# Performance work log

Measured on AMD Instinct MI355X. Metric: run time of the kernel, lower is better.

The kernel has to match this reference:

```python
import jax, jax.numpy as jnp
import numpy as np

EPS = 1e-6
K = 16
TEMP = 1.0
RES_SCALE = 0.5
CLAMP_MAX = 50.0


def _knn_indices(x, k):
    # x: (B,N,3) -> idx (B,N,k), self excluded; squared dist preserves ordering
    sq = jnp.sum(x * x, axis=-1)                      # (B,N)
    d2 = sq[:, :, None] + sq[:, None, :] - 2.0 * jnp.einsum('bnd,bmd->bnm', x, x)
    N = x.shape[1]
    eye = jnp.eye(N, dtype=bool)
    d2 = jnp.where(eye[None], jnp.inf, d2)
    _, idx = jax.lax.top_k(-d2, k)
    return idx


def _gather(t, idx):
    # t: (B,N,...), idx: (B,N,k) -> (B,N,k,...)
    return jax.vmap(lambda tb, ib: tb[ib])(t, idx)


def _vn_linear(v, W):
    return jnp.einsum('bncd,oc->bnod', v, W)


def _edge_mlp(s, W1, b1, W2, b2, W3, b3):
    h = jax.nn.silu(s @ W1.T + b1)
    h = jax.nn.silu(h @ W2.T + b2)
    return h @ W3.T + b3


def _vn_layer_norm(x, gamma, beta):
    norm = jnp.maximum(jnp.linalg.norm(x, axis=-1), EPS)      # (B,N,C)
    mean = jnp.mean(norm, axis=-1, keepdims=True)
    std = jnp.maximum(jnp.std(norm, axis=-1, keepdims=True, ddof=1), EPS)
    norm_scaled = (norm - mean) / std * gamma + beta
    return x / norm[..., None] * jnp.maximum(norm_scaled[..., None], EPS)


def _clamp_features(x, max_norm):
    n = jnp.maximum(jnp.linalg.norm(x, axis=-1, keepdims=True), EPS)
    scale = jnp.minimum(max_norm / n, 1.0)
    return x * scale


def setup_inputs() -> dict:
    key = jax.random.key(0)
    ks = jax.random.split(key, 12)
    B, N, C, Cout, H = 8, 2048, 128, 128, 32
    gain = 0.5
    lim = gain * np.sqrt(6.0 / (C + Cout))
    inp = {
        'x': jax.random.normal(ks[0], (B, N, 3), jnp.float32),
        'v': jax.random.normal(ks[1], (B, N, C, 3), jnp.float32),
        'Wq': jax.random.uniform(ks[2], (Cout, C), jnp.float32, -lim, lim),
        'Wk': jax.random.uniform(ks[3], (Cout, C), jnp.float32, -lim, lim),
        'Wu': jax.random.uniform(ks[4], (Cout, C), jnp.float32, -lim, lim),
        'W1': jax.random.normal(ks[5], (H, 4), jnp.float32) * 0.3,
        'b1': jnp.zeros((H,), jnp.float32),
        'W2': jax.random.normal(ks[6], (H, H), jnp.float32) * 0.15,
        'b2': jnp.zeros((H,), jnp.float32),
        'W3': jax.random.normal(ks[7], (1, H), jnp.float32) * 0.15,
        'b3': jnp.zeros((1,), jnp.float32),
        'gamma': jnp.ones((Cout,), jnp.float32),
        'beta': jnp.zeros((Cout,), jnp.float32),
    }
    return inp


def reference(x, v, Wq, Wk, Wu, W1, b1, W2, b2, W3, b3, gamma, beta):
    idx = _knn_indices(jax.lax.stop_gradient(x), K)           # (B,N,k)
    x_nbr = _gather(x, idx)                                    # (B,N,k,3)
    Q = _vn_linear(v, Wq)                                      # (B,N,Co,3)
    Kt = _vn_linear(v, Wk)
    U = _vn_linear(v, Wu)
    K_nbr = _gather(Kt, idx)                                   # (B,N,k,Co,3)
    U_nbr = _gather(U, idx)
    qn = jnp.mean(jnp.linalg.norm(Q, axis=-1), axis=-1, keepdims=True)   # (B,N,1)
    kn = jnp.mean(jnp.linalg.norm(Kt, axis=-1), axis=-1, keepdims=True)
    kn_nbr = _gather(kn, idx)                                  # (B,N,k,1)
    dot_nbr = jnp.mean(jnp.sum(Q[:, :, None] * K_nbr, axis=-1), axis=-1, keepdims=True)  # (B,N,k,1)
    dist = jnp.linalg.norm(x[:, :, None] - x_nbr, axis=-1, keepdims=True)                # (B,N,k,1)
    qn_exp = jnp.broadcast_to(qn[:, :, None], kn_nbr.shape)
    edge_s = jnp.concatenate([qn_exp, kn_nbr, dot_nbr, dist], axis=-1)   # (B,N,k,4)
    logits = jnp.clip(_edge_mlp(edge_s, W1, b1, W2, b2, W3, b3) / TEMP, -10.0, 10.0)
    attn = jax.nn.softmax(logits, axis=2)                      # (B,N,k,1)
    msg = jnp.sum(attn[..., None] * U_nbr, axis=2)             # (B,N,Co,3)
    out = Q + RES_SCALE * msg
    out = _vn_layer_norm(out, gamma, beta)
    out = _clamp_features(out, CLAMP_MAX)
    return out
```

## Files before the change

kernel.cpp:

```cpp
#include <hip/hip_runtime.h>
#include <math.h>

#define BB 8
#define NN 2048
#define CC 128
#define KNB 16
#define BN (BB*NN)
#define WPAD 136

#define EMPTYK 0xFFFFFFFFFFFFFFFFULL

typedef __attribute__((ext_vector_type(8))) short short8;
typedef __attribute__((ext_vector_type(4))) float floatx4;
typedef __attribute__((ext_vector_type(4), aligned(4))) float floatx4u;

__device__ __forceinline__ float silu_f(float x) {
  const float e = __builtin_amdgcn_exp2f(-1.442695040888963f * x);
  return x * __builtin_amdgcn_rcpf(1.0f + e);
}
__device__ __forceinline__ float fsqrt(float x) { return __builtin_amdgcn_sqrtf(x); }
__device__ __forceinline__ float frcp(float x)  { return __builtin_amdgcn_rcpf(x); }

__device__ __forceinline__ unsigned long long umin64(unsigned long long a, unsigned long long b) {
  return (b < a) ? b : a;
}

__device__ __forceinline__ unsigned short f2bf(float f) {
  unsigned u = __float_as_uint(f);
  unsigned r = u + 0x7FFFu + ((u >> 16) & 1u);
  return (unsigned short)(r >> 16);
}
__device__ __forceinline__ float bf2f(unsigned short s) {
  return __uint_as_float(((unsigned)s) << 16);
}

__device__ __forceinline__ float dot8(const float* __restrict__ w, const float* __restrict__ h) {
  const float4 a = *(const float4*)w;
  const float4 b = *(const float4*)(w + 4);
  float s = a.x*h[0];
  s = fmaf(a.y, h[1], s); s = fmaf(a.z, h[2], s); s = fmaf(a.w, h[3], s);
  s = fmaf(b.x, h[4], s); s = fmaf(b.y, h[5], s); s = fmaf(b.z, h[6], s);
  s = fmaf(b.w, h[7], s);
  return s;
}

__global__ __launch_bounds__(256) void knn_kernel(const float* __restrict__ x,
                                                  int* __restrict__ idx) {
  const int lane = threadIdx.x & 63;
  const int wave = threadIdx.x >> 6;
  const int bn = blockIdx.x * 4 + wave;
  const int b = bn >> 11;
  const int n = bn & (NN - 1);

  const float* xb = x + (size_t)b * NN * 3;
  const double xn0 = (double)xb[n*3+0], xn1 = (double)xb[n*3+1], xn2 = (double)xb[n*3+2];
  const double sqn = xn0*xn0 + xn1*xn1 + xn2*xn2;

  unsigned long long k[32];
  unsigned long long t0 = EMPTYK, t1 = EMPTYK, t2 = EMPTYK, t3 = EMPTYK;

  #pragma unroll
  for (int i = 0; i < 32; ++i) {
    const int m = i*64 + lane;
    const double a0 = (double)xb[m*3+0], a1 = (double)xb[m*3+1], a2 = (double)xb[m*3+2];
    const double sqm = a0*a0 + a1*a1 + a2*a2;
    const double dot = xn0*a0 + xn1*a1 + xn2*a2;
    const double d = sqn + sqm - 2.0*dot;
    unsigned long long kk =
        ((unsigned long long)__double_as_longlong(d) & ~2047ULL) | (unsigned long long)m;
    if (m == n) kk = 0x8000000000000000ULL | (unsigned long long)m;
    k[i] = kk;
    const bool l3 = kk < t3, l2 = kk < t2, l1 = kk < t1, l0 = kk < t0;
    t3 = l3 ? (l2 ? t2 : kk) : t3;
    t2 = l2 ? (l1 ? t1 : kk) : t2;
    t1 = l1 ? (l0 ? t0 : kk) : t1;
    t0 = l0 ? kk : t0;
  }

  int* op = idx + (size_t)bn * KNB;
  for (int t = 0; t < KNB; ++t) {
    unsigned long long g = t0;
    #pragma unroll
    for (int off = 32; off > 0; off >>= 1)
      g = umin64(g, (unsigned long long)__shfl_xor((unsigned long long)g, off, 64));

    if (lane == 0) op[t] = (int)(g & 2047ULL);

    const bool own = (t0 == g);
    t0 = own ? t1 : t0;
    t1 = own ? t2 : t1;
    t2 = own ? t3 : t2;
    t3 = own ? EMPTYK : t3;

    const bool need = (t0 == EMPTYK);
    if (__any(need)) {
      unsigned long long nm = EMPTYK;
      #pragma unroll
      for (int i = 0; i < 32; ++i) {
        const unsigned long long c = (k[i] > g) ? k[i] : EMPTYK;
        nm = umin64(nm, c);
      }
      t0 = need ? nm : t0;
    }
  }
}

__global__ __launch_bounds__(256) void wconv_kernel(
    const float* __restrict__ Wq, const float* __restrict__ Wk, const float* __restrict__ Wu,
    unsigned short* __restrict__ Whl)
{
  const int i = blockIdx.x*256 + threadIdx.x;
  const int mat = i >> 14, rem = i & 16383;
  const float* W = (mat == 0) ? Wq : ((mat == 1) ? Wk : Wu);
  const float f = W[rem];
  const unsigned short h = f2bf(f);
  const float r = f - bf2f(h);
  unsigned short* base = Whl + (size_t)mat * 2 * CC * CC;
  base[rem]           = h;
  base[CC*CC + rem]   = f2bf(r);
}

__global__ __launch_bounds__(256, 2) void vn_gemm_mfma(
    const float* __restrict__ v, const unsigned short* __restrict__ Whl,
    float* __restrict__ Q, float* __restrict__ Kt, float* __restrict__ U)
{
  __shared__ short Wh[CC][WPAD];
  __shared__ short Wl[CC][WPAD];

  const int tid  = threadIdx.x;
  const int lane = tid & 63;
  const int wave = tid >> 6;
  const int quad = lane >> 4;
  const int l15  = lane & 15;

  const int m = blockIdx.x*64 + wave*16 + l15;
  const int p = m / 3, d = m - 3*p;
  const float* vb = v + (size_t)p * (CC*3) + d;
  float areg[32];
  #pragma unroll
  for (int kc = 0; kc < 4; ++kc)
    #pragma unroll
    for (int j = 0; j < 8; ++j)
      areg[kc*8+j] = vb[(kc*32 + quad*8 + j)*3];

  short8 ah[4], al[4];
  #pragma unroll
  for (int kc = 0; kc < 4; ++kc)
    #pragma unroll
    for (int j = 0; j < 8; ++j) {
      const float f = areg[kc*8+j];
      unsigned short h = f2bf(f);
      float r = f - bf2f(h);
      ah[kc][j] = (short)h;
      al[kc][j] = (short)f2bf(r);
    }

  const int r0s = blockIdx.x*64 + wave*16 + quad*4;
  int pbase[4];
  #pragma unroll
  for (int reg = 0; reg < 4; ++reg) {
    const int r = r0s + reg;
    const int pp = r / 3;
    pbase[reg] = pp * (CC*3) + (r - 3*pp);
  }
  const int l153 = l15 * 3;

  for (int mat = 0; mat < 3; ++mat) {
    float* __restrict__ Out = (mat == 0) ? Q : ((mat == 1) ? Kt : U);
    const unsigned short* Wg = Whl + (size_t)mat * 2 * CC * CC;

    #pragma unroll
    for (int it = 0; it < 8; ++it) {
      const int i = it*256 + tid;
      const int o = i >> 4, c8 = (i & 15) * 8;
      *(short8*)&Wh[o][c8] = *(const short8*)&Wg[o*CC + c8];
      *(short8*)&Wl[o][c8] = *(const short8*)&Wg[CC*CC + o*CC + c8];
    }
    __syncthreads();

    floatx4 acc[8];
    #pragma unroll
    for (int ct = 0; ct < 8; ++ct) acc[ct] = (floatx4){0.f, 0.f, 0.f, 0.f};

    #pragma unroll
    for (int kc = 0; kc < 4; ++kc) {
      #pragma unroll
      for (int ct = 0; ct < 8; ++ct) {
        const int o = ct*16 + l15;
        const short8 bh = *(const short8*)&Wh[o][kc*32 + quad*8];
        const short8 bl = *(const short8*)&Wl[o][kc*32 + quad*8];
        acc[ct] = __builtin_amdgcn_mfma_f32_16x16x32_bf16(ah[kc], bh, acc[ct], 0, 0, 0);
        acc[ct] = __builtin_amdgcn_mfma_f32_16x16x32_bf16(al[kc], bh, acc[ct], 0, 0, 0);
        acc[ct] = __builtin_amdgcn_mfma_f32_16x16x32_bf16(ah[kc], bl, acc[ct], 0, 0, 0);
      }
    }
    __syncthreads();

    #pragma unroll
    for (int ct = 0; ct < 8; ++ct) {
      const int o3 = ct*48 + l153;
      #pragma unroll
      for (int reg = 0; reg < 4; ++reg)
        Out[pbase[reg] + o3] = acc[ct][reg];
    }
  }
}

__global__ __launch_bounds__(256) void kn_kernel(const float* __restrict__ Kt,
                                                 float* __restrict__ kn) {
  const int lane = threadIdx.x & 63;
  const int wave = threadIdx.x >> 6;
  const int bn = blockIdx.x * 4 + wave;
  const float* Kp = Kt + (size_t)bn * (CC*3) + lane*6;
  const floatx4u a = *(const floatx4u*)Kp;
  const float2 c = *(const float2*)(Kp+4);
  float s = fsqrt(a.x*a.x + a.y*a.y + a.z*a.z) + fsqrt(a.w*a.w + c.x*c.x + c.y*c.y);
  #pragma unroll
  for (int off = 1; off < 64; off <<= 1) s += __shfl_xor(s, off, 64);
  if (lane == 0) kn[bn] = s * (1.0f/128.0f);
}

__global__ __launch_bounds__(256) void attn_wave_kernel(
    const float* __restrict__ x, const int* __restrict__ idx,
    const float* __restrict__ Q, const float* __restrict__ Kt, const float* __restrict__ U,
    const float* __restrict__ kn,
    const float* __restrict__ W1, const float* __restrict__ b1,
    const float* __restrict__ W2, const float* __restrict__ b2,
    const float* __restrict__ W3, const float* __restrict__ b3,
    const float* __restrict__ gam, const float* __restrict__ bet,
    float* __restrict__ out)
{
  const int lane = threadIdx.x & 63;
  const int wv   = threadIdx.x >> 6;
  const int bn = ((blockIdx.x & 7) << 11) | (((blockIdx.x >> 3) << 2) | wv);
  const int b = bn >> 11;

  const float* Qp = Q + (size_t)bn * (CC*3) + lane*6;
  const floatx4u q0 = *(const floatx4u*)Qp;
  const float2 q1 = *(const float2*)(Qp+4);
  const float2 qa = make_float2(q0.x, q0.y);
  const float2 qb = make_float2(q0.z, q0.w);
  const float2 qc = make_float2(q1.x, q1.y);

  const int* ip = idx + (size_t)bn * KNB;
  int j[KNB];
  #pragma unroll
  for (int t = 0; t < KNB; ++t) j[t] = ip[t];

  const int kk = lane & 15;
  int jsel = j[0];
  #pragma unroll
  for (int t = 1; t < KNB; ++t) jsel = (kk == t) ? j[t] : jsel;

  const float xi0 = x[(size_t)bn*3+0], xi1 = x[(size_t)bn*3+1], xi2 = x[(size_t)bn*3+2];
  const float* xj = x + (size_t)(b*NN + jsel)*3;
  const float xj0 = xj[0], xj1 = xj[1], xj2 = xj[2];
  const float s1 = kn[(size_t)b*NN + jsel];

  float dpart[KNB];
  #pragma unroll
  for (int t = 0; t < KNB; ++t) {
    const float* Kp = Kt + (size_t)(b*NN + j[t]) * (CC*3) + lane*6;
    const floatx4u kv = *(const floatx4u*)Kp;
    const float2 kw = *(const float2*)(Kp+4);
    dpart[t] = qa.x*kv.x + qa.y*kv.y + qb.x*kv.z + qb.y*kv.w + qc.x*kw.x + qc.y*kw.y;
  }
  float qnp = fsqrt(qa.x*qa.x + qa.y*qa.y + qb.x*qb.x) + fsqrt(qb.y*qb.y + qc.x*qc.x + qc.y*qc.y);

  #pragma unroll
  for (int off = 1; off < 64; off <<= 1) qnp += __shfl_xor(qnp, off, 64);
  const float s0 = qnp * (1.0f/128.0f);

  float d8[8];
  {
    const bool hb = (lane & 1) != 0;
    #pragma unroll
    for (int t = 0; t < 8; ++t) {
      const float keep = hb ? dpart[2*t+1] : dpart[2*t];
      const float send = hb ? dpart[2*t]   : dpart[2*t+1];
      d8[t] = keep + __shfl_xor(send, 1, 64);
    }
  }
  float d4[4];
  {
    const bool hb = (lane & 2) != 0;
    #pragma unroll
    for (int t = 0; t < 4; ++t) {
      const float keep = hb ? d8[2*t+1] : d8[2*t];
      const float send = hb ? d8[2*t]   : d8[2*t+1];
      d4[t] = keep + __shfl_xor(send, 2, 64);
    }
  }
  float d2[2];
  {
    const bool hb = (lane & 4) != 0;
    #pragma unroll
    for (int t = 0; t < 2; ++t) {
      const float keep = hb ? d4[2*t+1] : d4[2*t];
      const float send = hb ? d4[2*t]   : d4[2*t+1];
      d2[t] = keep + __shfl_xor(send, 4, 64);
    }
  }
  float dsel;
  {
    const bool hb = (lane & 8) != 0;
    const float keep = hb ? d2[1] : d2[0];
    const float send = hb ? d2[0] : d2[1];
    dsel = keep + __shfl_xor(send, 8, 64);
  }
  dsel += __shfl_xor(dsel, 16, 64);
  dsel += __shfl_xor(dsel, 32, 64);

  const float dx = xi0 - xj0, dy = xi1 - xj1, dz = xi2 - xj2;
  const float s3 = fsqrt(dx*dx + dy*dy + dz*dz);
  const float s2 = dsel * (1.0f/128.0f);

  float u0[KNB], u1[KNB], u2[KNB], u3[KNB], u4[KNB], u5[KNB];
  #pragma unroll
  for (int t = 0; t < KNB; ++t) {
    const float* Up = U + (size_t)(b*NN + j[t]) * (CC*3) + lane*6;
    const floatx4u uv = *(const floatx4u*)Up;
    const float2 uw = *(const float2*)(Up+4);
    u0[t]=uv.x; u1[t]=uv.y; u2[t]=uv.z; u3[t]=uv.w; u4[t]=uw.x; u5[t]=uw.y;
  }

  const int g = lane >> 4;
  const int o0 = g*8, o1 = (g^1)*8, o2 = (g^2)*8, o3 = (g^3)*8;

  float h1o[8];
  {
    const float4 b1a = *(const float4*)(b1 + o0);
    const float4 b1b = *(const float4*)(b1 + o0 + 4);
    const float bb1[8] = {b1a.x,b1a.y,b1a.z,b1a.w,b1b.x,b1b.y,b1b.z,b1b.w};
    #pragma unroll
    for (int jj = 0; jj < 8; ++jj) {
      const float4 w = *(const float4*)(W1 + (o0 + jj)*4);
      float u = bb1[jj];
      u = fmaf(w.x, s0, u); u = fmaf(w.y, s1, u);
      u = fmaf(w.z, s2, u); u = fmaf(w.w, s3, u);
      h1o[jj] = silu_f(u);
    }
  }
  float hx16[8], hx32[8], hx48[8];
  #pragma unroll
  for (int jj = 0; jj < 8; ++jj) hx16[jj] = __shfl_xor(h1o[jj], 16, 64);
  #pragma unroll
  for (int jj = 0; jj < 8; ++jj) hx32[jj] = __shfl_xor(h1o[jj], 32, 64);
  #pragma unroll
  for (int jj = 0; jj < 8; ++jj) hx48[jj] = __shfl_xor(hx16[jj], 32, 64);

  float logit;
  {
    const float4 b2a = *(const float4*)(b2 + o0);
    const float4 b2b = *(const float4*)(b2 + o0 + 4);
    const float bb2[8] = {b2a.x,b2a.y,b2a.z,b2a.w,b2b.x,b2b.y,b2b.z,b2b.w};
    const float4 w3a = *(const float4*)(W3 + o0);
    const float4 w3b = *(const float4*)(W3 + o0 + 4);
    const float ww3[8] = {w3a.x,w3a.y,w3a.z,w3a.w,w3b.x,w3b.y,w3b.z,w3b.w};
    float lp = 0.f;
    #pragma unroll
    for (int hh = 0; hh < 8; ++hh) {
      const float* wr = W2 + (o0 + hh)*32;
      float a = bb2[hh];
      a += dot8(wr + o0, h1o);
      a += dot8(wr + o1, hx16);
      a += dot8(wr + o2, hx32);
      a += dot8(wr + o3, hx48);
      lp = fmaf(ww3[hh], silu_f(a), lp);
    }
    lp += __shfl_xor(lp, 16, 64);
    lp += __shfl_xor(lp, 32, 64);
    logit = lp + b3[0];
  }
  logit = fminf(fmaxf(logit, -10.0f), 10.0f);

  float mx = logit;
  #pragma unroll
  for (int off = 8; off > 0; off >>= 1) mx = fmaxf(mx, __shfl_xor(mx, off, 16));
  const float e = __builtin_amdgcn_exp2f(1.442695040888963f * (logit - mx));
  float ssum = e;
  #pragma unroll
  for (int off = 8; off > 0; off >>= 1) ssum += __shfl_xor(ssum, off, 16);
  const float w = e * frcp(ssum);

  float wk[KNB];
  #pragma unroll
  for (int t = 0; t < KNB; ++t) wk[t] = __shfl(w, t, 64);

  float m0=0.f,m1=0.f,m2=0.f,m3=0.f,m4=0.f,m5=0.f;
  #pragma unroll
  for (int t = 0; t < KNB; ++t) {
    const float ww = wk[t];
    m0 = fmaf(ww, u0[t], m0); m1 = fmaf(ww, u1[t], m1); m2 = fmaf(ww, u2[t], m2);
    m3 = fmaf(ww, u3[t], m3); m4 = fmaf(ww, u4[t], m4); m5 = fmaf(ww, u5[t], m5);
  }
  const float oa0 = qa.x + 0.5f*m0, oa1 = qa.y + 0.5f*m1, oa2 = qb.x + 0.5f*m2;
  const float ob0 = qb.y + 0.5f*m3, ob1 = qc.x + 0.5f*m4, ob2 = qc.y + 0.5f*m5;

  const float na = fmaxf(fsqrt(oa0*oa0 + oa1*oa1 + oa2*oa2), 1e-6f);
  const float nb = fmaxf(fsqrt(ob0*ob0 + ob1*ob1 + ob2*ob2), 1e-6f);
  float s = na + nb;
  #pragma unroll
  for (int off = 1; off < 64; off <<= 1) s += __shfl_xor(s, off, 64);
  const float mean = s * (1.0f/128.0f);
  const float dva = na - mean, dvb = nb - mean;
  float s2v = dva*dva + dvb*dvb;
  #pragma unroll
  for (int off = 1; off < 64; off <<= 1) s2v += __shfl_xor(s2v, off, 64);
  const float stdv = fmaxf(fsqrt(s2v * (1.0f/127.0f)), 1e-6f);
  const float rstd = frcp(stdv);

  const float2 gm = *(const float2*)(gam + lane*2);
  const float2 bt = *(const float2*)(bet + lane*2);
  const float nsa = (na - mean) * rstd * gm.x + bt.x;
  const float nsb = (nb - mean) * rstd * gm.y + bt.y;
  const float sca = fmaxf(nsa, 1e-6f) * frcp(na);
  const float scb = fmaxf(nsb, 1e-6f) * frcp(nb);
  float fa0 = oa0*sca, fa1 = oa1*sca, fa2 = oa2*sca;
  float fb0 = ob0*scb, fb1 = ob1*scb, fb2 = ob2*scb;
  const float n2a = fmaxf(fsqrt(fa0*fa0 + fa1*fa1 + fa2*fa2), 1e-6f);
  const float n2b = fmaxf(fsqrt(fb0*fb0 + fb1*fb1 + fb2*fb2), 1e-6f);
  const float c2a = fminf(50.0f * frcp(n2a), 1.0f);
  const float c2b = fminf(50.0f * frcp(n2b), 1.0f);

  float* op = out + (size_t)bn * (CC*3) + lane*6;
  floatx4u o4; o4.x = fa0*c2a; o4.y = fa1*c2a; o4.z = fa2*c2a; o4.w = fb0*c2b;
  *(floatx4u*)op = o4;
  *(float2*)(op+4) = make_float2(fb1*c2b, fb2*c2b);
}

extern "C" void kernel_launch(void* const* d_in, const int* in_sizes, int n_in,
                              void* d_out, int out_size, void* d_ws, size_t ws_size,
                              hipStream_t stream) {
  (void)in_sizes; (void)n_in; (void)out_size; (void)ws_size;
  const float* x   = (const float*)d_in[0];
  const float* v   = (const float*)d_in[1];
  const float* Wq  = (const float*)d_in[2];
  const float* Wk  = (const float*)d_in[3];
  const float* Wu  = (const float*)d_in[4];
  const float* W1  = (const float*)d_in[5];
  const float* b1  = (const float*)d_in[6];
  const float* W2  = (const float*)d_in[7];
  const float* b2  = (const float*)d_in[8];
  const float* W3  = (const float*)d_in[9];
  const float* b3  = (const float*)d_in[10];
  const float* gam = (const float*)d_in[11];
  const float* bet = (const float*)d_in[12];
  float* out = (float*)d_out;

  char* ws = (char*)d_ws;
  int*   idx = (int*)ws;
  float* Q   = (float*)(ws + (size_t)BN * KNB * 4);
  float* Kt  = Q  + (size_t)BN * CC * 3;
  float* U   = Kt + (size_t)BN * CC * 3;
  unsigned short* Whl = (unsigned short*)(U + (size_t)BN * CC * 3);
  float* kn  = (float*)((char*)Whl + (size_t)3 * 2 * CC * CC * 2);

  knn_kernel<<<BN/4, 256, 0, stream>>>(x, idx);
  wconv_kernel<<<192, 256, 0, stream>>>(Wq, Wk, Wu, Whl);
  vn_gemm_mfma<<<(BN*3)/64, 256, 0, stream>>>(v, Whl, Q, Kt, U);
  kn_kernel<<<BN/4, 256, 0, stream>>>(Kt, kn);
  attn_wave_kernel<<<BN/4, 256, 0, stream>>>(x, idx, Q, Kt, U, kn,
                                             W1, b1, W2, b2, W3, b3, gam, bet, out);
}
```

Baseline: 279.3 us.

## Split attention into logits and message kernels, fuse kn into logits, cheapen knn argmin

Removes the standalone kn kernel and instead computes neighbor key norms on the fly from the K rows already loaded for the dot products. The attention kernel is split in two: one computes softmax weights into a workspace array, the other gathers U and does the weighted sum plus layer norm. This lowers register pressure from holding 96 U values per lane. The knn top-k selection replaces the 64-bit shuffle min with a 32-bit high-word reduction plus a ballot, and only falls back to a low-word reduction when the high words tie. In exchange, Q and idx are read twice and the weights take an extra global round trip.

```diff
diff --git a/kernel.cpp b/kernel.cpp
--- a/kernel.cpp
+++ b/kernel.cpp
@@ -79,14 +79,33 @@
 
   int* op = idx + (size_t)bn * KNB;
   for (int t = 0; t < KNB; ++t) {
-    unsigned long long g = t0;
-    #pragma unroll
-    for (int off = 32; off > 0; off >>= 1)
-      g = umin64(g, (unsigned long long)__shfl_xor((unsigned long long)g, off, 64));
-
-    if (lane == 0) op[t] = (int)(g & 2047ULL);
-
-    const bool own = (t0 == g);
+    const unsigned h0 = (unsigned)(t0 >> 32);
+    const unsigned l0w = (unsigned)t0;
+    unsigned hm = h0;
+    #pragma unroll
+    for (int off = 32; off > 0; off >>= 1) {
+      const unsigned o = (unsigned)__shfl_xor((int)hm, off, 64);
+      hm = (o < hm) ? o : hm;
+    }
+    const bool tied = (h0 == hm);
+    const unsigned long long bal = __ballot(tied);
+    unsigned lm;
+    if (__builtin_popcountll(bal) == 1) {
+      const int owner = __builtin_ctzll(bal);
+      lm = (unsigned)__shfl((int)l0w, owner, 64);
+    } else {
+      lm = tied ? l0w : 0xFFFFFFFFu;
+      #pragma unroll
+      for (int off = 32; off > 0; off >>= 1) {
+        const unsigned o = (unsigned)__shfl_xor((int)lm, off, 64);
+        lm = (o < lm) ? o : lm;
+      }
+    }
+    const unsigned long long g = ((unsigned long long)hm << 32) | (unsigned long long)lm;
+
+    if (lane == 0) op[t] = (int)(lm & 2047u);
+
+    const bool own = tied && (l0w == lm);
     t0 = own ? t1 : t0;
     t1 = own ? t2 : t1;
     t2 = own ? t3 : t2;
@@ -206,29 +225,13 @@
   }
 }
 
-__global__ __launch_bounds__(256) void kn_kernel(const float* __restrict__ Kt,
-                                                 float* __restrict__ kn) {
-  const int lane = threadIdx.x & 63;
-  const int wave = threadIdx.x >> 6;
-  const int bn = blockIdx.x * 4 + wave;
-  const float* Kp = Kt + (size_t)bn * (CC*3) + lane*6;
-  const floatx4u a = *(const floatx4u*)Kp;
-  const float2 c = *(const float2*)(Kp+4);
-  float s = fsqrt(a.x*a.x + a.y*a.y + a.z*a.z) + fsqrt(a.w*a.w + c.x*c.x + c.y*c.y);
-  #pragma unroll
-  for (int off = 1; off < 64; off <<= 1) s += __shfl_xor(s, off, 64);
-  if (lane == 0) kn[bn] = s * (1.0f/128.0f);
-}
-
-__global__ __launch_bounds__(256) void attn_wave_kernel(
+__global__ __launch_bounds__(256) void attn_logits_kernel(
     const float* __restrict__ x, const int* __restrict__ idx,
-    const float* __restrict__ Q, const float* __restrict__ Kt, const float* __restrict__ U,
-    const float* __restrict__ kn,
+    const float* __restrict__ Q, const float* __restrict__ Kt,
     const float* __restrict__ W1, const float* __restrict__ b1,
     const float* __restrict__ W2, const float* __restrict__ b2,
     const float* __restrict__ W3, const float* __restrict__ b3,
-    const float* __restrict__ gam, const float* __restrict__ bet,
-    float* __restrict__ out)
+    float* __restrict__ warr)
 {
   const int lane = threadIdx.x & 63;
   const int wv   = threadIdx.x >> 6;
@@ -255,15 +258,15 @@
   const float xi0 = x[(size_t)bn*3+0], xi1 = x[(size_t)bn*3+1], xi2 = x[(size_t)bn*3+2];
   const float* xj = x + (size_t)(b*NN + jsel)*3;
   const float xj0 = xj[0], xj1 = xj[1], xj2 = xj[2];
-  const float s1 = kn[(size_t)b*NN + jsel];
-
-  float dpart[KNB];
+
+  float dpart[KNB], knp[KNB];
   #pragma unroll
   for (int t = 0; t < KNB; ++t) {
     const float* Kp = Kt + (size_t)(b*NN + j[t]) * (CC*3) + lane*6;
     const floatx4u kv = *(const floatx4u*)Kp;
     const float2 kw = *(const float2*)(Kp+4);
     dpart[t] = qa.x*kv.x + qa.y*kv.y + qb.x*kv.z + qb.y*kv.w + qc.x*kw.x + qc.y*kw.y;
+    knp[t] = fsqrt(kv.x*kv.x + kv.y*kv.y + kv.z*kv.z) + fsqrt(kv.w*kv.w + kw.x*kw.x + kw.y*kw.y);
   }
   float qnp = fsqrt(qa.x*qa.x + qa.y*qa.y + qb.x*qb.x) + fsqrt(qb.y*qb.y + qc.x*qc.x + qc.y*qc.y);
 
@@ -271,58 +274,67 @@
   for (int off = 1; off < 64; off <<= 1) qnp += __shfl_xor(qnp, off, 64);
   const float s0 = qnp * (1.0f/128.0f);
 
-  float d8[8];
+  float d8[8], k8[8];
   {
     const bool hb = (lane & 1) != 0;
     #pragma unroll
     for (int t = 0; t < 8; ++t) {
-      const float keep = hb ? dpart[2*t+1] : dpart[2*t];
-      const float send = hb ? dpart[2*t]   : dpart[2*t+1];
-      d8[t] = keep + __shfl_xor(send, 1, 64);
-    }
-  }
-  float d4[4];
+      const float dk = hb ? dpart[2*t+1] : dpart[2*t];
+      const float dsn = hb ? dpart[2*t]  : dpart[2*t+1];
+      const float kv = hb ? knp[2*t+1]   : knp[2*t];
+      const float ksn = hb ? knp[2*t]    : knp[2*t+1];
+      d8[t] = dk + __shfl_xor(dsn, 1, 64);
+      k8[t] = kv + __shfl_xor(ksn, 1, 64);
+    }
+  }
+  float d4[4], k4[4];
   {
     const bool hb = (lane & 2) != 0;
     #pragma unroll
     for (int t = 0; t < 4; ++t) {
-      const float keep = hb ? d8[2*t+1] : d8[2*t];
-      const float send = hb ? d8[2*t]   : d8[2*t+1];
-      d4[t] = keep + __shfl_xor(send, 2, 64);
-    }
-  }
-  float d2[2];
+      const float dk = hb ? d8[2*t+1] : d8[2*t];
+      const float dsn = hb ? d8[2*t]  : d8[2*t+1];
+      const float kv = hb ? k8[2*t+1] : k8[2*t];
+      const float ksn = hb ? k8[2*t]  : k8[2*t+1];
+      d4[t] = dk + __shfl_xor(dsn, 2, 64);
+      k4[t] = kv + __shfl_xor(ksn, 2, 64);
+    }
+  }
+  float d2a, d2b, k2a, k2b;
   {
     const bool hb = (lane & 4) != 0;
-    #pragma unroll
-    for (int t = 0; t < 2; ++t) {
-      const float keep = hb ? d4[2*t+1] : d4[2*t];
-      const float send = hb ? d4[2*t]   : d4[2*t+1];
-      d2[t] = keep + __shfl_xor(send, 4, 64);
-    }
-  }
-  float dsel;
+    const float dk0 = hb ? d4[1] : d4[0];
+    const float dsn0 = hb ? d4[0] : d4[1];
+    const float dk1 = hb ? d4[3] : d4[2];
+    const float dsn1 = hb ? d4[2] : d4[3];
+    d2a = dk0 + __shfl_xor(dsn0, 4, 64);
+    d2b = dk1 + __shfl_xor(dsn1, 4, 64);
+    const float kk0 = hb ? k4[1] : k4[0];
+    const float ksn0 = hb ? k4[0] : k4[1];
+    const float kk1 = hb ? k4[3] : k4[2];
+    const float ksn1 = hb ? k4[2] : k4[3];
+    k2a = kk0 + __shfl_xor(ksn0, 4, 64);
+    k2b = kk1 + __shfl_xor(ksn1, 4, 64);
+  }
+  float dsel, knsel;
   {
     const bool hb = (lane & 8) != 0;
-    const float keep = hb ? d2[1] : d2[0];
-    const float send = hb ? d2[0] : d2[1];
-    dsel = keep + __shfl_xor(send, 8, 64);
-  }
-  dsel += __shfl_xor(dsel, 16, 64);
-  dsel += __shfl_xor(dsel, 32, 64);
+    const float dk = hb ? d2b : d2a;
+    const float dsn = hb ? d2a : d2b;
+    dsel = dk + __shfl_xor(dsn, 8, 64);
+    const float kv = hb ? k2b : k2a;
+    const float ksn = hb ? k2a : k2b;
+    knsel = kv + __shfl_xor(ksn, 8, 64);
+  }
+  dsel  += __shfl_xor(dsel, 16, 64);
+  dsel  += __shfl_xor(dsel, 32, 64);
+  knsel += __shfl_xor(knsel, 16, 64);
+  knsel += __shfl_xor(knsel, 32, 64);
 
   const float dx = xi0 - xj0, dy = xi1 - xj1, dz = xi2 - xj2;
   const float s3 = fsqrt(dx*dx + dy*dy + dz*dz);
+  const float s1 = knsel * (1.0f/128.0f);
   const float s2 = dsel * (1.0f/128.0f);
-
-  float u0[KNB], u1[KNB], u2[KNB], u3[KNB], u4[KNB], u5[KNB];
-  #pragma unroll
-  for (int t = 0; t < KNB; ++t) {
-    const float* Up = U + (size_t)(b*NN + j[t]) * (CC*3) + lane*6;
-    const floatx4u uv = *(const floatx4u*)Up;
-    const float2 uw = *(const float2*)(Up+4);
-    u0[t]=uv.x; u1[t]=uv.y; u2[t]=uv.z; u3[t]=uv.w; u4[t]=uw.x; u5[t]=uw.y;
-  }
 
   const int g = lane >> 4;
   const int o0 = g*8, o1 = (g^1)*8, o2 = (g^2)*8, o3 = (g^3)*8;
@@ -383,19 +395,46 @@
   for (int off = 8; off > 0; off >>= 1) ssum += __shfl_xor(ssum, off, 16);
   const float w = e * frcp(ssum);
 
+  if (lane < KNB) warr[(size_t)bn * KNB + lane] = w;
+}
+
+__global__ __launch_bounds__(256) void attn_msg_kernel(
+    const int* __restrict__ idx, const float* __restrict__ Q,
+    const float* __restrict__ U, const float* __restrict__ warr,
+    const float* __restrict__ gam, const float* __restrict__ bet,
+    float* __restrict__ out)
+{
+  const int lane = threadIdx.x & 63;
+  const int wv   = threadIdx.x >> 6;
+  const int bn = ((blockIdx.x & 7) << 11) | (((blockIdx.x >> 3) << 2) | wv);
+  const int b = bn >> 11;
+
+  const float* Qp = Q + (size_t)bn * (CC*3) + lane*6;
+  const floatx4u q0 = *(const floatx4u*)Qp;
+  const float2 q1 = *(const float2*)(Qp+4);
+
+  const int* ip = idx + (size_t)bn * KNB;
+  int j[KNB];
+  #pragma unroll
+  for (int t = 0; t < KNB; ++t) j[t] = ip[t];
+
+  const float* wp = warr + (size_t)bn * KNB;
   float wk[KNB];
   #pragma unroll
-  for (int t = 0; t < KNB; ++t) wk[t] = __shfl(w, t, 64);
+  for (int t = 0; t < KNB; ++t) wk[t] = wp[t];
 
   float m0=0.f,m1=0.f,m2=0.f,m3=0.f,m4=0.f,m5=0.f;
   #pragma unroll
   for (int t = 0; t < KNB; ++t) {
+    const float* Up = U + (size_t)(b*NN + j[t]) * (CC*3) + lane*6;
+    const floatx4u uv = *(const floatx4u*)Up;
+    const float2 uw = *(const float2*)(Up+4);
     const float ww = wk[t];
-    m0 = fmaf(ww, u0[t], m0); m1 = fmaf(ww, u1[t], m1); m2 = fmaf(ww, u2[t], m2);
-    m3 = fmaf(ww, u3[t], m3); m4 = fmaf(ww, u4[t], m4); m5 = fmaf(ww, u5[t], m5);
-  }
-  const float oa0 = qa.x + 0.5f*m0, oa1 = qa.y + 0.5f*m1, oa2 = qb.x + 0.5f*m2;
-  const float ob0 = qb.y + 0.5f*m3, ob1 = qc.x + 0.5f*m4, ob2 = qc.y + 0.5f*m5;
+    m0 = fmaf(ww, uv.x, m0); m1 = fmaf(ww, uv.y, m1); m2 = fmaf(ww, uv.z, m2);
+    m3 = fmaf(ww, uv.w, m3); m4 = fmaf(ww, uw.x, m4); m5 = fmaf(ww, uw.y, m5);
+  }
+  const float oa0 = q0.x + 0.5f*m0, oa1 = q0.y + 0.5f*m1, oa2 = q0.z + 0.5f*m2;
+  const float ob0 = q0.w + 0.5f*m3, ob1 = q1.x + 0.5f*m4, ob2 = q1.y + 0.5f*m5;
 
   const float na = fmaxf(fsqrt(oa0*oa0 + oa1*oa1 + oa2*oa2), 1e-6f);
   const float nb = fmaxf(fsqrt(ob0*ob0 + ob1*ob1 + ob2*ob2), 1e-6f);
@@ -454,12 +493,12 @@
   float* Kt  = Q  + (size_t)BN * CC * 3;
   float* U   = Kt + (size_t)BN * CC * 3;
   unsigned short* Whl = (unsigned short*)(U + (size_t)BN * CC * 3);
-  float* kn  = (float*)((char*)Whl + (size_t)3 * 2 * CC * CC * 2);
+  float* warr = (float*)((char*)Whl + (size_t)3 * 2 * CC * CC * 2);
 
   knn_kernel<<<BN/4, 256, 0, stream>>>(x, idx);
   wconv_kernel<<<192, 256, 0, stream>>>(Wq, Wk, Wu, Whl);
   vn_gemm_mfma<<<(BN*3)/64, 256, 0, stream>>>(v, Whl, Q, Kt, U);
-  kn_kernel<<<BN/4, 256, 0, stream>>>(Kt, kn);
-  attn_wave_kernel<<<BN/4, 256, 0, stream>>>(x, idx, Q, Kt, U, kn,
-                                             W1, b1, W2, b2, W3, b3, gam, bet, out);
-}
+  attn_logits_kernel<<<BN/4, 256, 0, stream>>>(x, idx, Q, Kt,
+                                               W1, b1, W2, b2, W3, b3, warr);
+  attn_msg_kernel<<<BN/4, 256, 0, stream>>>(idx, Q, U, warr, gam, bet, out);
+}
```

After: 266.2 us. 4.7% less time.

## Split attention kernel, precompute point norms, and cheapen KNN 64-bit argmin

Applied to the files above, without the earlier changes.

Splits the fused attention kernel into a logits kernel that writes softmax weights to a workspace and a message kernel that gathers U and applies layer norm. This is meant to cut register pressure from holding 96 U values across the edge MLP. KNN now reads padded float4 points and precomputed double squared norms from a new sq_kernel. Its per-step 64-bit wave reduction becomes a 32-bit high-word min plus a ballot, with a low-word reduction only on ties. The trade-off is two extra launches and extra global traffic for the weights, Q and idx.

```diff
diff --git a/kernel.cpp b/kernel.cpp
--- a/kernel.cpp
+++ b/kernel.cpp
@@ -44,7 +44,18 @@
   return s;
 }
 
-__global__ __launch_bounds__(256) void knn_kernel(const float* __restrict__ x,
+__global__ __launch_bounds__(256) void sq_kernel(const float* __restrict__ x,
+                                                 double* __restrict__ sqd,
+                                                 float4* __restrict__ x4) {
+  const int i = blockIdx.x*256 + threadIdx.x;
+  const float f0 = x[i*3+0], f1 = x[i*3+1], f2 = x[i*3+2];
+  const double a0 = (double)f0, a1 = (double)f1, a2 = (double)f2;
+  sqd[i] = a0*a0 + a1*a1 + a2*a2;
+  x4[i] = make_float4(f0, f1, f2, 0.0f);
+}
+
+__global__ __launch_bounds__(256) void knn_kernel(const float4* __restrict__ x4,
+                                                  const double* __restrict__ sqd,
                                                   int* __restrict__ idx) {
   const int lane = threadIdx.x & 63;
   const int wave = threadIdx.x >> 6;
@@ -52,9 +63,11 @@
   const int b = bn >> 11;
   const int n = bn & (NN - 1);
 
-  const float* xb = x + (size_t)b * NN * 3;
-  const double xn0 = (double)xb[n*3+0], xn1 = (double)xb[n*3+1], xn2 = (double)xb[n*3+2];
-  const double sqn = xn0*xn0 + xn1*xn1 + xn2*xn2;
+  const float4* xb4 = x4 + (size_t)b * NN;
+  const double* sqb = sqd + (size_t)b * NN;
+  const float4 xq = xb4[n];
+  const double xn0 = (double)xq.x, xn1 = (double)xq.y, xn2 = (double)xq.z;
+  const double sqn = sqb[n];
 
   unsigned long long k[32];
   unsigned long long t0 = EMPTYK, t1 = EMPTYK, t2 = EMPTYK, t3 = EMPTYK;
@@ -62,8 +75,9 @@
   #pragma unroll
   for (int i = 0; i < 32; ++i) {
     const int m = i*64 + lane;
-    const double a0 = (double)xb[m*3+0], a1 = (double)xb[m*3+1], a2 = (double)xb[m*3+2];
-    const double sqm = a0*a0 + a1*a1 + a2*a2;
+    const float4 xm = xb4[m];
+    const double a0 = (double)xm.x, a1 = (double)xm.y, a2 = (double)xm.z;
+    const double sqm = sqb[m];
     const double dot = xn0*a0 + xn1*a1 + xn2*a2;
     const double d = sqn + sqm - 2.0*dot;
     unsigned long long kk =
@@ -79,14 +93,33 @@
 
   int* op = idx + (size_t)bn * KNB;
   for (int t = 0; t < KNB; ++t) {
-    unsigned long long g = t0;
-    #pragma unroll
-    for (int off = 32; off > 0; off >>= 1)
-      g = umin64(g, (unsigned long long)__shfl_xor((unsigned long long)g, off, 64));
-
-    if (lane == 0) op[t] = (int)(g & 2047ULL);
-
-    const bool own = (t0 == g);
+    const unsigned h0 = (unsigned)(t0 >> 32);
+    const unsigned l0w = (unsigned)t0;
+    unsigned hm = h0;
+    #pragma unroll
+    for (int off = 32; off > 0; off >>= 1) {
+      const unsigned o = (unsigned)__shfl_xor((int)hm, off, 64);
+      hm = (o < hm) ? o : hm;
+    }
+    const bool tied = (h0 == hm);
+    const unsigned long long bal = __ballot(tied);
+    unsigned lm;
+    if (__builtin_popcountll(bal) == 1) {
+      const int owner = __builtin_ctzll(bal);
+      lm = (unsigned)__shfl((int)l0w, owner, 64);
+    } else {
+      lm = tied ? l0w : 0xFFFFFFFFu;
+      #pragma unroll
+      for (int off = 32; off > 0; off >>= 1) {
+        const unsigned o = (unsigned)__shfl_xor((int)lm, off, 64);
+        lm = (o < lm) ? o : lm;
+      }
+    }
+    const unsigned long long g = ((unsigned long long)hm << 32) | (unsigned long long)lm;
+
+    if (lane == 0) op[t] = (int)(lm & 2047u);
+
+    const bool own = tied && (l0w == lm);
     t0 = own ? t1 : t0;
     t1 = own ? t2 : t1;
     t2 = own ? t3 : t2;
@@ -212,23 +245,23 @@
   const int wave = threadIdx.x >> 6;
   const int bn = blockIdx.x * 4 + wave;
   const float* Kp = Kt + (size_t)bn * (CC*3) + lane*6;
-  const floatx4u a = *(const floatx4u*)Kp;
-  const float2 c = *(const float2*)(Kp+4);
-  float s = fsqrt(a.x*a.x + a.y*a.y + a.z*a.z) + fsqrt(a.w*a.w + c.x*c.x + c.y*c.y);
+  const floatx4u kv = *(const floatx4u*)Kp;
+  const float2 kw = *(const float2*)(Kp+4);
+  float s = fsqrt(kv.x*kv.x + kv.y*kv.y + kv.z*kv.z)
+          + fsqrt(kv.w*kv.w + kw.x*kw.x + kw.y*kw.y);
   #pragma unroll
   for (int off = 1; off < 64; off <<= 1) s += __shfl_xor(s, off, 64);
   if (lane == 0) kn[bn] = s * (1.0f/128.0f);
 }
 
-__global__ __launch_bounds__(256) void attn_wave_kernel(
+__global__ __launch_bounds__(256) void attn_logits_kernel(
     const float* __restrict__ x, const int* __restrict__ idx,
-    const float* __restrict__ Q, const float* __restrict__ Kt, const float* __restrict__ U,
+    const float* __restrict__ Q, const float* __restrict__ Kt,
     const float* __restrict__ kn,
     const float* __restrict__ W1, const float* __restrict__ b1,
     const float* __restrict__ W2, const float* __restrict__ b2,
     const float* __restrict__ W3, const float* __restrict__ b3,
-    const float* __restrict__ gam, const float* __restrict__ bet,
-    float* __restrict__ out)
+    float* __restrict__ warr)
 {
   const int lane = threadIdx.x & 63;
   const int wv   = threadIdx.x >> 6;
@@ -314,15 +347,6 @@
   const float dx = xi0 - xj0, dy = xi1 - xj1, dz = xi2 - xj2;
   const float s3 = fsqrt(dx*dx + dy*dy + dz*dz);
   const float s2 = dsel * (1.0f/128.0f);
-
-  float u0[KNB], u1[KNB], u2[KNB], u3[KNB], u4[KNB], u5[KNB];
-  #pragma unroll
-  for (int t = 0; t < KNB; ++t) {
-    const float* Up = U + (size_t)(b*NN + j[t]) * (CC*3) + lane*6;
-    const floatx4u uv = *(const floatx4u*)Up;
-    const float2 uw = *(const float2*)(Up+4);
-    u0[t]=uv.x; u1[t]=uv.y; u2[t]=uv.z; u3[t]=uv.w; u4[t]=uw.x; u5[t]=uw.y;
-  }
 
   const int g = lane >> 4;
   const int o0 = g*8, o1 = (g^1)*8, o2 = (g^2)*8, o3 = (g^3)*8;
@@ -383,19 +407,46 @@
   for (int off = 8; off > 0; off >>= 1) ssum += __shfl_xor(ssum, off, 16);
   const float w = e * frcp(ssum);
 
+  if (lane < KNB) warr[(size_t)bn * KNB + lane] = w;
+}
+
+__global__ __launch_bounds__(256) void attn_msg_kernel(
+    const int* __restrict__ idx, const float* __restrict__ Q,
+    const float* __restrict__ U, const float* __restrict__ warr,
+    const float* __restrict__ gam, const float* __restrict__ bet,
+    float* __restrict__ out)
+{
+  const int lane = threadIdx.x & 63;
+  const int wv   = threadIdx.x >> 6;
+  const int bn = ((blockIdx.x & 7) << 11) | (((blockIdx.x >> 3) << 2) | wv);
+  const int b = bn >> 11;
+
+  const int* ip = idx + (size_t)bn * KNB;
+  int j[KNB];
+  #pragma unroll
+  for (int t = 0; t < KNB; ++t) j[t] = ip[t];
+
+  const float* Qp = Q + (size_t)bn * (CC*3) + lane*6;
+  const floatx4u q0 = *(const floatx4u*)Qp;
+  const float2 q1 = *(const float2*)(Qp+4);
+
+  const float* wp = warr + (size_t)bn * KNB;
   float wk[KNB];
   #pragma unroll
-  for (int t = 0; t < KNB; ++t) wk[t] = __shfl(w, t, 64);
+  for (int t = 0; t < KNB; ++t) wk[t] = wp[t];
 
   float m0=0.f,m1=0.f,m2=0.f,m3=0.f,m4=0.f,m5=0.f;
   #pragma unroll
   for (int t = 0; t < KNB; ++t) {
+    const float* Up = U + (size_t)(b*NN + j[t]) * (CC*3) + lane*6;
+    const floatx4u uv = *(const floatx4u*)Up;
+    const float2 uw = *(const float2*)(Up+4);
     const float ww = wk[t];
-    m0 = fmaf(ww, u0[t], m0); m1 = fmaf(ww, u1[t], m1); m2 = fmaf(ww, u2[t], m2);
-    m3 = fmaf(ww, u3[t], m3); m4 = fmaf(ww, u4[t], m4); m5 = fmaf(ww, u5[t], m5);
-  }
-  const float oa0 = qa.x + 0.5f*m0, oa1 = qa.y + 0.5f*m1, oa2 = qb.x + 0.5f*m2;
-  const float ob0 = qb.y + 0.5f*m3, ob1 = qc.x + 0.5f*m4, ob2 = qc.y + 0.5f*m5;
+    m0 = fmaf(ww, uv.x, m0); m1 = fmaf(ww, uv.y, m1); m2 = fmaf(ww, uv.z, m2);
+    m3 = fmaf(ww, uv.w, m3); m4 = fmaf(ww, uw.x, m4); m5 = fmaf(ww, uw.y, m5);
+  }
+  const float oa0 = q0.x + 0.5f*m0, oa1 = q0.y + 0.5f*m1, oa2 = q0.z + 0.5f*m2;
+  const float ob0 = q0.w + 0.5f*m3, ob1 = q1.x + 0.5f*m4, ob2 = q1.y + 0.5f*m5;
 
   const float na = fmaxf(fsqrt(oa0*oa0 + oa1*oa1 + oa2*oa2), 1e-6f);
   const float nb = fmaxf(fsqrt(ob0*ob0 + ob1*ob1 + ob2*ob2), 1e-6f);
@@ -454,12 +505,17 @@
   float* Kt  = Q  + (size_t)BN * CC * 3;
   float* U   = Kt + (size_t)BN * CC * 3;
   unsigned short* Whl = (unsigned short*)(U + (size_t)BN * CC * 3);
-  float* kn  = (float*)((char*)Whl + (size_t)3 * 2 * CC * CC * 2);
-
-  knn_kernel<<<BN/4, 256, 0, stream>>>(x, idx);
+  float* warr = (float*)((char*)Whl + (size_t)3 * 2 * CC * CC * 2);
+  double* sqd = (double*)(warr + (size_t)BN * KNB);
+  float4* x4  = (float4*)(sqd + (size_t)BN);
+  float*  kn  = (float*)(x4 + (size_t)BN);
+
+  sq_kernel<<<BN/256, 256, 0, stream>>>(x, sqd, x4);
+  knn_kernel<<<BN/4, 256, 0, stream>>>(x4, sqd, idx);
   wconv_kernel<<<192, 256, 0, stream>>>(Wq, Wk, Wu, Whl);
   vn_gemm_mfma<<<(BN*3)/64, 256, 0, stream>>>(v, Whl, Q, Kt, U);
   kn_kernel<<<BN/4, 256, 0, stream>>>(Kt, kn);
-  attn_wave_kernel<<<BN/4, 256, 0, stream>>>(x, idx, Q, Kt, U, kn,
-                                             W1, b1, W2, b2, W3, b3, gam, bet, out);
-}
+  attn_logits_kernel<<<BN/4, 256, 0, stream>>>(x, idx, Q, Kt, kn,
+                                               W1, b1, W2, b2, W3, b3, warr);
+  attn_msg_kernel<<<BN/4, 256, 0, stream>>>(idx, Q, U, warr, gam, bet, out);
+}
```

After: 282.6 us. No clear change (+1.2%).
